# Optimization experiments

Measured on AMD Instinct MI355X. Metric: run time of the kernel, lower is better.

## Reference

```python
import jax, jax.numpy as jnp
import numpy as np

N_SAMPLES = 32768
DAMPING = 0.9998
EPS = 1e-8


def sim(home, tensions, masses, gains, mics, forces, home_modifier):
    # forces, home_modifier: (B, M, D, T); home: (1,1,D,1)
    B, M, D, T = forces.shape
    h = home + home_modifier                          # (B,M,D,T)
    f_t = jnp.moveaxis(forces, -1, 0)                 # (T,B,M,D)
    h_t = jnp.moveaxis(h, -1, 0)                      # (T,B,M,D)

    def step(carry, xs):
        pos, vel = carry
        f, hh = xs
        direction = hh - pos
        acc = f + tensions * direction / masses
        vel = (vel + acc) * DAMPING
        pos = pos + vel
        # mic readout: tanh(vel*gains) dotted with mics over dim
        r = jnp.sum(jnp.tanh(vel * gains) * mics, axis=-1)  # (B,M)
        return (pos, vel), (r, direction)

    init = (jnp.zeros((B, M, D), forces.dtype), jnp.zeros((B, M, D), forces.dtype))
    _, (rec, disp) = jax.lax.scan(step, init, (f_t, h_t))
    recording = jnp.moveaxis(rec, 0, -1)              # (B,M,T)
    displacement = jnp.moveaxis(disp, 0, -1)          # (B,M,D,T)
    return recording, displacement


def interpolate_last_axis(x, size):
    # linear interpolation along last axis (F.interpolate mode='linear', align_corners=False)
    T = x.shape[-1]
    pos = jnp.clip((jnp.arange(size) + 0.5) * (T / size) - 0.5, 0.0, T - 1)
    i0 = jnp.floor(pos).astype(jnp.int32)
    i1 = jnp.minimum(i0 + 1, T - 1)
    w = (pos - i0).astype(x.dtype)
    return x[..., i0] * (1 - w) + x[..., i1] * w


def fft_resample(x, desired):
    # zero-pad spectrum to upsample
    spec = jnp.fft.rfft(x, axis=-1, norm='ortho')
    n_coeffs = desired // 2 + 1
    new = jnp.zeros(x.shape[:-1] + (n_coeffs,), dtype=spec.dtype)
    new = new.at[..., :spec.shape[-1]].set(spec)
    return jnp.fft.irfft(new, n=desired, axis=-1, norm='ortho')


def fft_convolve(a, b):
    # linear convolution via 2N-padded FFT, truncated to N
    n = a.shape[-1]
    pa = jnp.pad(a, [(0, 0)] * (a.ndim - 1) + [(0, n)])
    pb = jnp.pad(b, [(0, 0)] * (b.ndim - 1) + [(0, b.shape[-1])])
    spec = jnp.fft.rfft(pa, axis=-1) * jnp.fft.rfft(pb, axis=-1)
    return jnp.fft.irfft(spec, axis=-1)[..., :n]


def forward(forces, home_modifier, filters, home, masses, tensions, gains, mics, to_filter_mixture):
    recording, displacement = sim(home, tensions, masses, gains, mics, forces, home_modifier)
    mixture = jnp.einsum('bmdt,df->bmft', displacement, to_filter_mixture)
    mixture = interpolate_last_axis(mixture, N_SAMPLES)               # (B,M,F,S)
    upsampled = fft_resample(recording, N_SAMPLES)                    # (B,M,S)
    noise = jax.random.uniform(jax.random.key(1), upsampled.shape,
                               dtype=upsampled.dtype, minval=-1.0, maxval=1.0)
    upsampled = jnp.abs(upsampled) * noise
    f = jnp.pad(filters, ((0, 0), (0, 0), (0, N_SAMPLES - filters.shape[-1])))[:, None, :, :]  # (B,1,F,S)
    f = f / (jnp.linalg.norm(f, axis=-1, keepdims=True) + EPS)
    filtered = fft_convolve(f, upsampled[:, :, None, :])              # (B,M,F,S)
    hf = jnp.einsum('bmfs,bmfs->bms', mixture, filtered) + upsampled  # (B,M,S)
    return recording, displacement, hf


def setup_inputs():
    key = jax.random.key(0)
    ks = jax.random.split(key, 8)
    B, M, D, T, F_, L = 2, 32, 64, 2048, 16, 512
    return {
        'forces': jax.random.normal(ks[0], (B, M, D, T), jnp.float32) * 0.01,
        'home_modifier': jax.random.normal(ks[1], (B, M, D, T), jnp.float32),
        'filters': jax.random.normal(ks[2], (B, F_, L), jnp.float32),
        'home': jnp.zeros((1, 1, D, 1), jnp.float32),
        'masses': jax.random.uniform(ks[3], (1, M, 1), jnp.float32, 1000.0, 10000.0),
        'tensions': jax.random.uniform(ks[4], (1, M, D), jnp.float32, 20.0, 30.0),
        'gains': jax.random.uniform(ks[5], (1, M, 1), jnp.float32, 10.0, 100.0),
        'mics': jax.random.uniform(ks[6], (1, M, D), jnp.float32, -1.0, 1.0),
        'to_filter_mixture': jax.random.uniform(ks[7], (D, F_), jnp.float32, -1.0, 1.0),
    }


def reference(forces, home_modifier, filters, home, masses, tensions, gains, mics, to_filter_mixture):
    return forward(forces, home_modifier, filters, home, masses, tensions, gains, mics, to_filter_mixture)
```

## Files before the change

### kernel.cpp

```cpp
#include <hip/hip_runtime.h>
#include <cstdint>
#include <cstddef>

#define DAMP 0.9998f

typedef __attribute__((ext_vector_type(8))) short bf16x8;
typedef __attribute__((ext_vector_type(4))) float f32x4;

__device__ __forceinline__ unsigned short f2bf(float x) {
    unsigned u = __float_as_uint(x);
    unsigned r = (u + 0x7FFFu + ((u >> 16) & 1u)) >> 16;
    return (unsigned short)r;
}
__device__ __forceinline__ float bf2f(unsigned short v) {
    return __uint_as_float((unsigned)v << 16);
}

__device__ __forceinline__ void threefry_0j(unsigned j, unsigned& o0, unsigned& o1) {
    unsigned x0 = 0u;
    unsigned x1 = j + 1u;
    const unsigned ks2 = 0x1BD11BDBu;
#define TFR(r) { x0 += x1; x1 = (x1 << (r)) | (x1 >> (32 - (r))); x1 ^= x0; }
    TFR(13) TFR(15) TFR(26) TFR(6)
    x0 += 1u;   x1 += ks2 + 1u;
    TFR(17) TFR(29) TFR(16) TFR(24)
    x0 += ks2;  x1 += 0u + 2u;
    TFR(13) TFR(15) TFR(26) TFR(6)
       x1 += 1u + 3u;
    TFR(17) TFR(29) TFR(16) TFR(24)
    x0 += 1u;   x1 += ks2 + 4u;
    TFR(13) TFR(15) TFR(26) TFR(6)
    x0 += ks2;  x1 += 0u + 5u;
#undef TFR
    o0 = x0; o1 = x1;
}

__device__ __forceinline__ float noise_at(unsigned j) {
    unsigned o0, o1;
    threefry_0j(j, o0, o1);
    unsigned bits = o0 ^ o1;
    float u = __uint_as_float((bits >> 9) | 0x3F800000u) - 1.0f;
    return fmaxf(-1.0f, u * 2.0f - 1.0f);
}

__device__ __forceinline__ float dir_val(unsigned u) {
    if (u == 0u) return 2049.f;
    const float PIO = 9.58737992e-05f;
    unsigned y = (2049u * u) & 65535u;
    float sgn = 1.f;
    if (y >= 32768u) { y -= 32768u; sgn = -1.f; }
    unsigned yy = (y > 16384u) ? (32768u - y) : y;
    float sy = sgn * sinf((float)yy * PIO);
    unsigned uu = (u > 16384u) ? (32768u - u) : u;
    float su = sinf((float)uu * PIO);
    return sy / su;
}

__global__ void tables_kernel(const float* __restrict__ filters,
                              unsigned short* __restrict__ dirrev,
                              unsigned short* __restrict__ fnrev) {
    const int tid = threadIdx.x;
    if (blockIdx.x < 128) {
        const unsigned i = blockIdx.x * 256 + tid;
        const unsigned p = i >> 11, k = i & 2047u;
        dirrev[i] = f2bf(dir_val(16u * (2047u - k) + p));
    } else if (tid < 64) {
        const int row = blockIdx.x - 128;
        const float* src = filters + (size_t)row * 512;
        float s = 0.f;
        for (int i = tid; i < 512; i += 64) { const float v = src[i]; s += v * v; }
        #pragma unroll
        for (int off = 32; off; off >>= 1) s += __shfl_xor(s, off);
        const float scale = 1.f / (sqrtf(s) + 1e-8f);
        for (int i = tid; i < 512; i += 64)
            fnrev[(size_t)row * 512 + i] = f2bf(src[511 - i] * scale);
    }
}

__global__ __launch_bounds__(64) void sim_pass1(const float* __restrict__ forces,
                                                const float* __restrict__ hmod,
                                                const float* __restrict__ home,
                                                const float* __restrict__ masses,
                                                const float* __restrict__ tensions,
                                                float* __restrict__ w) {
    const int blk = blockIdx.x;
    const int bm = blk >> 6, c = blk & 63;
    const int m = bm & 31;
    const int d = threadIdx.x;
    const int t0 = c * 32;
    __shared__ float kv[64];
    __shared__ float hv[64];
    __shared__ __align__(16) float gt[64][33];
    kv[d] = tensions[m * 64 + d] / masses[m];
    hv[d] = home[d];
    __syncthreads();
    for (int i = d; i < 512; i += 64) {
        const int dd = i >> 3, q = (i & 7) * 4;
        const size_t off = ((size_t)bm * 64 + dd) * 2048 + t0 + q;
        const float4 fv = *(const float4*)(forces + off);
        const float4 hm = *(const float4*)(hmod + off);
        const float kk = kv[dd], hh = hv[dd];
        float4 g;
        g.x = fmaf(kk, hh + hm.x, fv.x);
        g.y = fmaf(kk, hh + hm.y, fv.y);
        g.z = fmaf(kk, hh + hm.z, fv.z);
        g.w = fmaf(kk, hh + hm.w, fv.w);
        *(float4*)&gt[dd][q] = g;
    }
    __syncthreads();
    const float k = kv[d];
    float pos = 0.f, vel = 0.f;
    #pragma unroll 8
    for (int ts = 0; ts < 32; ++ts) {
        const float acc = fmaf(-k, pos, gt[d][ts]);
        vel = (vel + acc) * DAMP;
        pos = pos + vel;
    }
    float* wrow = w + (size_t)blk * 128;
    wrow[d] = pos; wrow[64 + d] = vel;
}

__global__ __launch_bounds__(64) void sim_scan(const float* __restrict__ masses,
                                               const float* __restrict__ tensions,
                                               float* __restrict__ w) {
    const int bm = blockIdx.x;
    const int m = bm & 31;
    const int d = threadIdx.x;
    const double kd = (double)(tensions[m * 64 + d] / masses[m]);
    const double cd = (double)DAMP;
    double Ma = 1.0 - cd * kd, Mb = cd, Mc = -cd * kd, Md = cd;
    #pragma unroll
    for (int it = 0; it < 5; ++it) {
        const double na = Ma * Ma + Mb * Mc;
        const double nb = Ma * Mb + Mb * Md;
        const double nc = Mc * Ma + Md * Mc;
        const double nd = Mc * Mb + Md * Md;
        Ma = na; Mb = nb; Mc = nc; Md = nd;
    }
    double pos = 0.0, vel = 0.0;
    float* wb = w + (size_t)bm * 64 * 128;
    for (int c = 0; c < 64; ++c) {
        float* row = wb + c * 128;
        const double wp = (double)row[d];
        const double wv = (double)row[64 + d];
        row[d] = (float)pos;
        row[64 + d] = (float)vel;
        const double np = Ma * pos + Mb * vel + wp;
        const double nv = Mc * pos + Md * vel + wv;
        pos = np; vel = nv;
    }
}

__global__ __launch_bounds__(64) void sim_pass2(const float* __restrict__ forces,
                                                const float* __restrict__ hmod,
                                                const float* __restrict__ home,
                                                const float* __restrict__ masses,
                                                const float* __restrict__ tensions,
                                                const float* __restrict__ gains,
                                                const float* __restrict__ mics,
                                                const float* __restrict__ w,
                                                float* __restrict__ disp,
                                                float* __restrict__ rec) {
    const int blk = blockIdx.x;
    const int bm = blk >> 6, c = blk & 63;
    const int m = bm & 31;
    const int d = threadIdx.x;
    const int t0 = c * 32;
    __shared__ __align__(16) float ft[64][17];
    __shared__ __align__(16) float ht[64][17];
    const float k = tensions[m * 64 + d] / masses[m];
    const float gain = gains[m];
    const float mic = mics[m * 64 + d];
    const float hd = home[d];

    float pos = w[(size_t)blk * 128 + d];
    float vel = w[(size_t)blk * 128 + 64 + d];

    #pragma unroll
    for (int phase = 0; phase < 2; ++phase) {
        const int t0p = t0 + phase * 16;
        for (int i = d; i < 256; i += 64) {
            const int dd = i >> 2, q = (i & 3) * 4;
            const size_t off = ((size_t)bm * 64 + dd) * 2048 + t0p + q;
            *(float4*)&ft[dd][q] = *(const float4*)(forces + off);
            *(float4*)&ht[dd][q] = *(const float4*)(hmod + off);
        }
        __syncthreads();
        #pragma unroll
        for (int ts = 0; ts < 16; ++ts) {
            const float f = ft[d][ts];
            const float h = hd + ht[d][ts];
            const float dir = h - pos;
            const float acc = f + k * dir;
            vel = (vel + acc) * DAMP;
            pos = pos + vel;
            ft[d][ts] = dir;
            const float x = vel * gain;
            const float e = __expf(2.f * x);
            ht[d][ts] = (1.f - 2.f / (e + 1.f)) * mic;
        }
        __syncthreads();
        for (int i = d; i < 256; i += 64) {
            const int dd = i >> 2, q = (i & 3) * 4;
            const size_t off = ((size_t)bm * 64 + dd) * 2048 + t0p + q;
            *(float4*)(disp + off) = *(float4*)&ft[dd][q];
        }
        {
            const int ts = d & 15, part = d >> 4;
            float s = 0.f;
            #pragma unroll
            for (int j = 0; j < 16; ++j) s += ht[16 * part + j][ts];
            s += __shfl_xor(s, 16);
            s += __shfl_xor(s, 32);
            if (d < 16) rec[(size_t)bm * 2048 + t0p + d] = s;
        }
        __syncthreads();
    }
}

__global__ __launch_bounds__(256) void mix_kernel(const float* __restrict__ disp,
                                                  const float* __restrict__ tofm,
                                                  unsigned short* __restrict__ mixture) {
    __shared__ __align__(16) float tf[64][16];
    const int tid = threadIdx.x;
    for (int i = tid; i < 1024; i += 256) tf[i >> 4][i & 15] = tofm[i];
    __syncthreads();
    const int bm = blockIdx.y;
    const int t = blockIdx.x * 256 + tid;
    float acc[16];
    #pragma unroll
    for (int f = 0; f < 16; ++f) acc[f] = 0.f;
    for (int d = 0; d < 64; ++d) {
        const float v = disp[((size_t)bm * 64 + d) * 2048 + t];
        const float4* r4 = (const float4*)tf[d];
        const float4 a4 = r4[0], b4 = r4[1], c4 = r4[2], d4 = r4[3];
        acc[0]  += v * a4.x; acc[1]  += v * a4.y; acc[2]  += v * a4.z; acc[3]  += v * a4.w;
        acc[4]  += v * b4.x; acc[5]  += v * b4.y; acc[6]  += v * b4.z; acc[7]  += v * b4.w;
        acc[8]  += v * c4.x; acc[9]  += v * c4.y; acc[10] += v * c4.z; acc[11] += v * c4.w;
        acc[12] += v * d4.x; acc[13] += v * d4.y; acc[14] += v * d4.z; acc[15] += v * d4.w;
    }
    #pragma unroll
    for (int f = 0; f < 16; ++f)
        mixture[((size_t)bm * 16 + f) * 2048 + t] = f2bf(acc[f]);
}

#define DR_STRIDE 4112u
#define W_STRIDE  5136u
#define W_OFF     65792u
#define RS_SMEM   106880u

__global__ __launch_bounds__(256) void resample_kernel(const float* __restrict__ rec,
                                                       const unsigned short* __restrict__ dirrev,
                                                       float* __restrict__ up) {
    const int bm = blockIdx.x;
    const int Q0 = blockIdx.y * 512;
    const int tid = threadIdx.x;
    __shared__ __align__(16) unsigned char smem[RS_SMEM];

    for (int i = tid; i < 4096; i += 256) {
        const int p = i >> 8, c16 = i & 255;
        *(uint4*)(smem + (unsigned)p * DR_STRIDE + 16u * c16) = ((const uint4*)dirrev)[i];
    }
    for (int x = tid; x < 2560; x += 256) {
        const int g = (Q0 + x + 1) & 2047;
        const unsigned short bv = f2bf(rec[(size_t)bm * 2048 + g]);
        #pragma unroll
        for (int sg = 0; sg < 8; ++sg) {
            const int y = x - sg;
            if (y >= 0) *(unsigned short*)(smem + W_OFF + sg * W_STRIDE + 2 * y) = bv;
        }
    }
    __syncthreads();

    const int lane = tid & 63;
    const int wv = tid >> 6;
    const int i15 = lane & 15;
    const int g4 = lane >> 4;

    f32x4 acc[8];
    #pragma unroll
    for (int i = 0; i < 8; ++i) acc[i] = (f32x4){0.f, 0.f, 0.f, 0.f};

    const unsigned abase = (unsigned)i15 * DR_STRIDE + 16u * g4;
    const unsigned bbase = W_OFF + (unsigned)(i15 & 7) * W_STRIDE + 16u * (i15 >> 3) + 16u * g4;

    for (int kkb = 0; kkb < 8; ++kkb) {
        bf16x8 afr[8];
        #pragma unroll
        for (int kj = 0; kj < 8; ++kj)
            afr[kj] = *(const bf16x8*)(smem + abase + 64u * (kkb * 8 + kj));
        #pragma unroll
        for (int qtl = 0; qtl < 8; ++qtl) {
            const int qt = wv * 8 + qtl;
            const unsigned bb = bbase + 32u * qt;
            #pragma unroll
            for (int kj = 0; kj < 8; ++kj) {
                const bf16x8 bfr = *(const bf16x8*)(smem + bb + 64u * (kkb * 8 + kj));
                acc[qtl] = __builtin_amdgcn_mfma_f32_16x16x32_bf16(afr[kj], bfr, acc[qtl], 0, 0, 0);
            }
        }
    }

    #pragma unroll
    for (int qtl = 0; qtl < 8; ++qtl) {
        const int qt = wv * 8 + qtl;
        const int q = Q0 + 16 * qt + i15;
        const int sbase = 16 * q + 4 * g4;
        const unsigned jb = (unsigned)bm * 32768u + (unsigned)sbase;
        float4 o;
        o.x = fabsf(acc[qtl][0] * (1.f / 8192.f)) * noise_at(jb);
        o.y = fabsf(acc[qtl][1] * (1.f / 8192.f)) * noise_at(jb + 1u);
        o.z = fabsf(acc[qtl][2] * (1.f / 8192.f)) * noise_at(jb + 2u);
        o.w = fabsf(acc[qtl][3] * (1.f / 8192.f)) * noise_at(jb + 3u);
        *(float4*)(up + (size_t)bm * 32768 + sbase) = o;
    }
}

#define W_STR2   3088u
#define MX_OFF   24704u
#define HF_SMEM  26880u

__global__ __launch_bounds__(256) void hf_kernel(const float* __restrict__ up,
                                                 const unsigned short* __restrict__ fnrev,
                                                 const unsigned short* __restrict__ mixture,
                                                 float* __restrict__ hf) {
    const int tile = blockIdx.x;
    const int bm = blockIdx.y;
    const int b = bm >> 5;
    const int S0 = tile * 1024;
    const int tbase = tile * 64 - 1;
    const int tid = threadIdx.x;

    __shared__ __align__(16) unsigned char smem[HF_SMEM];
    unsigned short* mixl = (unsigned short*)(smem + MX_OFF);

    for (int x = tid; x < 1536; x += 256) {
        const int gidx = S0 - 511 + x;
        const float u = (gidx >= 0 && gidx < 32768) ? up[(size_t)bm * 32768 + gidx] : 0.f;
        const unsigned short v = f2bf(u);
        #pragma unroll
        for (int sg = 0; sg < 8; ++sg) {
            const int y = x - sg;
            if (y >= 0) *(unsigned short*)(smem + sg * W_STR2 + 2 * y) = v;
        }
    }
    for (int i = tid; i < 16 * 66; i += 256) {
        const int f = i / 66, tt = i - f * 66;
        const int t = tbase + tt;
        mixl[f * 68 + tt] = (t >= 0 && t < 2048)
            ? mixture[((size_t)bm * 16 + f) * 2048 + t] : (unsigned short)0;
    }
    const int lane = tid & 63;
    const int i15 = lane & 15;
    const int g4 = lane >> 4;
    const int wv = tid >> 6;
    bf16x8 afr[16];
    #pragma unroll
    for (int kk = 0; kk < 16; ++kk)
        afr[kk] = *(const bf16x8*)(fnrev + (size_t)(b * 16 + i15) * 512 + 32 * kk + 8 * g4);
    __syncthreads();

    for (int rr = 0; rr < 4; ++rr) {
        const int rho = wv * 4 + rr;
        const int sig = rho & 7;
        const unsigned baseR = (unsigned)sig * W_STR2 + 2u * (rho - sig)
                             + 32u * i15 + 16u * g4;
        #pragma unroll
        for (int g = 0; g < 4; ++g) {
            f32x4 acc = {0.f, 0.f, 0.f, 0.f};
            const unsigned tb = baseR + 512u * g;
            #pragma unroll
            for (int kk = 0; kk < 16; ++kk) {
                const bf16x8 bfr = *(const bf16x8*)(smem + tb + 64u * kk);
                acc = __builtin_amdgcn_mfma_f32_16x16x32_bf16(afr[kk], bfr, acc, 0, 0, 0);
            }
            const int s = S0 + 256 * g + rho + 16 * i15;
            float posf = ((float)s + 0.5f) * 0.0625f - 0.5f;
            posf = fminf(fmaxf(posf, 0.f), 2047.f);
            const int i0 = (int)posf;
            const float wg = posf - (float)i0;
            const int i1 = min(i0 + 1, 2047);
            const int t0 = i0 - tbase, t1 = i1 - tbase;
            float part = 0.f;
            #pragma unroll
            for (int r = 0; r < 4; ++r) {
                const int f = 4 * g4 + r;
                const float mv = bf2f(mixl[f * 68 + t0]) * (1.f - wg)
                               + bf2f(mixl[f * 68 + t1]) * wg;
                part += mv * acc[r];
            }
            part += __shfl_xor(part, 16);
            part += __shfl_xor(part, 32);
            if (g4 == 0) {
                const int e = 511 + 256 * g + rho + 16 * i15;
                const float upv = bf2f(*(const unsigned short*)(smem + 2 * e));
                hf[(size_t)bm * 32768 + s] = part + upv;
            }
        }
    }
}

extern "C" void kernel_launch(void* const* d_in, const int* in_sizes, int n_in,
                              void* d_out, int out_size, void* d_ws, size_t ws_size,
                              hipStream_t stream) {
    const float* forces   = (const float*)d_in[0];
    const float* hmod     = (const float*)d_in[1];
    const float* filters  = (const float*)d_in[2];
    const float* home     = (const float*)d_in[3];
    const float* masses   = (const float*)d_in[4];
    const float* tensions = (const float*)d_in[5];
    const float* gains    = (const float*)d_in[6];
    const float* mics     = (const float*)d_in[7];
    const float* tofm     = (const float*)d_in[8];

    float* out  = (float*)d_out;
    float* rec  = out;
    float* disp = out + 131072;
    float* hf   = out + 8519680;

    float* up               = (float*)d_ws;
    unsigned short* mixture = (unsigned short*)((float*)d_ws + 2097152);
    unsigned short* dirrev  = (unsigned short*)((float*)d_ws + 3145728);
    float* w                = (float*)d_ws + 3162112;
    unsigned short* fnrev   = (unsigned short*)((float*)d_ws + 3686400);

    tables_kernel<<<160, 256, 0, stream>>>(filters, dirrev, fnrev);
    sim_pass1<<<4096, 64, 0, stream>>>(forces, hmod, home, masses, tensions, w);
    sim_scan<<<64, 64, 0, stream>>>(masses, tensions, w);
    sim_pass2<<<4096, 64, 0, stream>>>(forces, hmod, home, masses, tensions, gains, mics, w, disp, rec);
    mix_kernel<<<dim3(8, 64), 256, 0, stream>>>(disp, tofm, mixture);
    resample_kernel<<<dim3(64, 4), 256, 0, stream>>>(rec, dirrev, up);
    hf_kernel<<<dim3(32, 64), 256, 0, stream>>>(up, fnrev, mixture, hf);
}
```

Before: 129.2 us.

## Fold table kernel into sim_pass1, halve resample smem, store upsampled as bf16

The separate tables kernel is removed and its work (the dirrev table and the normalized reversed filters) is done by extra blocks appended to sim_pass1, saving one launch. resample_kernel now stages the dirrev table in two K-halves, which cuts shared memory from about 107KB to 74KB and may allow more blocks per CU. The upsampled intermediate is written as bf16 instead of fp32, halving its write and read traffic, since hf_kernel converted it to bf16 anyway. The cost is an extra barrier per K-chunk in resample.

```diff
diff --git a/kernel.cpp b/kernel.cpp
--- a/kernel.cpp
+++ b/kernel.cpp
@@ -5,6 +5,7 @@
 #define DAMP 0.9998f
 
 typedef __attribute__((ext_vector_type(8))) short bf16x8;
+typedef __attribute__((ext_vector_type(4))) unsigned short u16x4;
 typedef __attribute__((ext_vector_type(4))) float f32x4;
 
 __device__ __forceinline__ unsigned short f2bf(float x) {
@@ -56,37 +57,37 @@
     return sy / su;
 }
 
-__global__ void tables_kernel(const float* __restrict__ filters,
-                              unsigned short* __restrict__ dirrev,
-                              unsigned short* __restrict__ fnrev) {
-    const int tid = threadIdx.x;
-    if (blockIdx.x < 128) {
-        const unsigned i = blockIdx.x * 256 + tid;
-        const unsigned p = i >> 11, k = i & 2047u;
-        dirrev[i] = f2bf(dir_val(16u * (2047u - k) + p));
-    } else if (tid < 64) {
-        const int row = blockIdx.x - 128;
-        const float* src = filters + (size_t)row * 512;
-        float s = 0.f;
-        for (int i = tid; i < 512; i += 64) { const float v = src[i]; s += v * v; }
-        #pragma unroll
-        for (int off = 32; off; off >>= 1) s += __shfl_xor(s, off);
-        const float scale = 1.f / (sqrtf(s) + 1e-8f);
-        for (int i = tid; i < 512; i += 64)
-            fnrev[(size_t)row * 512 + i] = f2bf(src[511 - i] * scale);
-    }
-}
-
 __global__ __launch_bounds__(64) void sim_pass1(const float* __restrict__ forces,
                                                 const float* __restrict__ hmod,
                                                 const float* __restrict__ home,
                                                 const float* __restrict__ masses,
                                                 const float* __restrict__ tensions,
-                                                float* __restrict__ w) {
+                                                float* __restrict__ w,
+                                                const float* __restrict__ filters,
+                                                unsigned short* __restrict__ dirrev,
+                                                unsigned short* __restrict__ fnrev) {
     const int blk = blockIdx.x;
+    const int d = threadIdx.x;
+    if (blk >= 4608) {
+        const int row = blk - 4608;
+        const float* src = filters + (size_t)row * 512;
+        float s = 0.f;
+        for (int i = d; i < 512; i += 64) { const float v = src[i]; s += v * v; }
+        #pragma unroll
+        for (int off = 32; off; off >>= 1) s += __shfl_xor(s, off);
+        const float scale = 1.f / (sqrtf(s) + 1e-8f);
+        for (int i = d; i < 512; i += 64)
+            fnrev[(size_t)row * 512 + i] = f2bf(src[511 - i] * scale);
+        return;
+    }
+    if (blk >= 4096) {
+        const unsigned i = (unsigned)(blk - 4096) * 64u + (unsigned)d;
+        const unsigned p = i >> 11, k = i & 2047u;
+        dirrev[i] = f2bf(dir_val(16u * (2047u - k) + p));
+        return;
+    }
     const int bm = blk >> 6, c = blk & 63;
     const int m = bm & 31;
-    const int d = threadIdx.x;
     const int t0 = c * 32;
     __shared__ float kv[64];
     __shared__ float hv[64];
@@ -244,23 +245,19 @@
         mixture[((size_t)bm * 16 + f) * 2048 + t] = f2bf(acc[f]);
 }
 
-#define DR_STRIDE 4112u
+#define DR_STRIDE 2064u
 #define W_STRIDE  5136u
-#define W_OFF     65792u
-#define RS_SMEM   106880u
+#define W_OFF     33024u
+#define RS_SMEM   74112u
 
 __global__ __launch_bounds__(256) void resample_kernel(const float* __restrict__ rec,
                                                        const unsigned short* __restrict__ dirrev,
-                                                       float* __restrict__ up) {
+                                                       unsigned short* __restrict__ upb) {
     const int bm = blockIdx.x;
     const int Q0 = blockIdx.y * 512;
     const int tid = threadIdx.x;
     __shared__ __align__(16) unsigned char smem[RS_SMEM];
 
-    for (int i = tid; i < 4096; i += 256) {
-        const int p = i >> 8, c16 = i & 255;
-        *(uint4*)(smem + (unsigned)p * DR_STRIDE + 16u * c16) = ((const uint4*)dirrev)[i];
-    }
     for (int x = tid; x < 2560; x += 256) {
         const int g = (Q0 + x + 1) & 2047;
         const unsigned short bv = f2bf(rec[(size_t)bm * 2048 + g]);
@@ -270,7 +267,6 @@
             if (y >= 0) *(unsigned short*)(smem + W_OFF + sg * W_STRIDE + 2 * y) = bv;
         }
     }
-    __syncthreads();
 
     const int lane = tid & 63;
     const int wv = tid >> 6;
@@ -284,19 +280,29 @@
     const unsigned abase = (unsigned)i15 * DR_STRIDE + 16u * g4;
     const unsigned bbase = W_OFF + (unsigned)(i15 & 7) * W_STRIDE + 16u * (i15 >> 3) + 16u * g4;
 
-    for (int kkb = 0; kkb < 8; ++kkb) {
-        bf16x8 afr[8];
-        #pragma unroll
-        for (int kj = 0; kj < 8; ++kj)
-            afr[kj] = *(const bf16x8*)(smem + abase + 64u * (kkb * 8 + kj));
-        #pragma unroll
-        for (int qtl = 0; qtl < 8; ++qtl) {
-            const int qt = wv * 8 + qtl;
-            const unsigned bb = bbase + 32u * qt;
+    for (int kc = 0; kc < 2; ++kc) {
+        if (kc) __syncthreads();
+        for (int i = tid; i < 2048; i += 256) {
+            const int p = i >> 7, c16 = i & 127;
+            *(uint4*)(smem + (unsigned)p * DR_STRIDE + 16u * c16) =
+                *(const uint4*)(dirrev + (size_t)p * 2048 + kc * 1024 + 8 * c16);
+        }
+        __syncthreads();
+
+        for (int kkb = 0; kkb < 4; ++kkb) {
+            bf16x8 afr[8];
             #pragma unroll
-            for (int kj = 0; kj < 8; ++kj) {
-                const bf16x8 bfr = *(const bf16x8*)(smem + bb + 64u * (kkb * 8 + kj));
-                acc[qtl] = __builtin_amdgcn_mfma_f32_16x16x32_bf16(afr[kj], bfr, acc[qtl], 0, 0, 0);
+            for (int kj = 0; kj < 8; ++kj)
+                afr[kj] = *(const bf16x8*)(smem + abase + 64u * (kkb * 8 + kj));
+            #pragma unroll
+            for (int qtl = 0; qtl < 8; ++qtl) {
+                const int qt = wv * 8 + qtl;
+                const unsigned bb = bbase + 32u * qt + 2048u * kc;
+                #pragma unroll
+                for (int kj = 0; kj < 8; ++kj) {
+                    const bf16x8 bfr = *(const bf16x8*)(smem + bb + 64u * (kkb * 8 + kj));
+                    acc[qtl] = __builtin_amdgcn_mfma_f32_16x16x32_bf16(afr[kj], bfr, acc[qtl], 0, 0, 0);
+                }
             }
         }
     }
@@ -307,12 +313,12 @@
         const int q = Q0 + 16 * qt + i15;
         const int sbase = 16 * q + 4 * g4;
         const unsigned jb = (unsigned)bm * 32768u + (unsigned)sbase;
-        float4 o;
-        o.x = fabsf(acc[qtl][0] * (1.f / 8192.f)) * noise_at(jb);
-        o.y = fabsf(acc[qtl][1] * (1.f / 8192.f)) * noise_at(jb + 1u);
-        o.z = fabsf(acc[qtl][2] * (1.f / 8192.f)) * noise_at(jb + 2u);
-        o.w = fabsf(acc[qtl][3] * (1.f / 8192.f)) * noise_at(jb + 3u);
-        *(float4*)(up + (size_t)bm * 32768 + sbase) = o;
+        u16x4 o;
+        o[0] = f2bf(fabsf(acc[qtl][0] * (1.f / 8192.f)) * noise_at(jb));
+        o[1] = f2bf(fabsf(acc[qtl][1] * (1.f / 8192.f)) * noise_at(jb + 1u));
+        o[2] = f2bf(fabsf(acc[qtl][2] * (1.f / 8192.f)) * noise_at(jb + 2u));
+        o[3] = f2bf(fabsf(acc[qtl][3] * (1.f / 8192.f)) * noise_at(jb + 3u));
+        *(u16x4*)(upb + (size_t)bm * 32768 + sbase) = o;
     }
 }
 
@@ -320,7 +326,7 @@
 #define MX_OFF   24704u
 #define HF_SMEM  26880u
 
-__global__ __launch_bounds__(256) void hf_kernel(const float* __restrict__ up,
+__global__ __launch_bounds__(256) void hf_kernel(const unsigned short* __restrict__ upb,
                                                  const unsigned short* __restrict__ fnrev,
                                                  const unsigned short* __restrict__ mixture,
                                                  float* __restrict__ hf) {
@@ -336,8 +342,8 @@
 
     for (int x = tid; x < 1536; x += 256) {
         const int gidx = S0 - 511 + x;
-        const float u = (gidx >= 0 && gidx < 32768) ? up[(size_t)bm * 32768 + gidx] : 0.f;
-        const unsigned short v = f2bf(u);
+        const unsigned short v = (gidx >= 0) ? upb[(size_t)bm * 32768 + gidx]
+                                             : (unsigned short)0;
         #pragma unroll
         for (int sg = 0; sg < 8; ++sg) {
             const int y = x - sg;
@@ -418,17 +424,17 @@
     float* disp = out + 131072;
     float* hf   = out + 8519680;
 
-    float* up               = (float*)d_ws;
-    unsigned short* mixture = (unsigned short*)((float*)d_ws + 2097152);
-    unsigned short* dirrev  = (unsigned short*)((float*)d_ws + 3145728);
-    float* w                = (float*)d_ws + 3162112;
-    unsigned short* fnrev   = (unsigned short*)((float*)d_ws + 3686400);
-
-    tables_kernel<<<160, 256, 0, stream>>>(filters, dirrev, fnrev);
-    sim_pass1<<<4096, 64, 0, stream>>>(forces, hmod, home, masses, tensions, w);
+    unsigned short* upb     = (unsigned short*)d_ws;
+    unsigned short* mixture = (unsigned short*)((float*)d_ws + 1048576);
+    unsigned short* dirrev  = (unsigned short*)((float*)d_ws + 2097152);
+    float* w                = (float*)d_ws + 2113536;
+    unsigned short* fnrev   = (unsigned short*)((float*)d_ws + 2637824);
+
+    sim_pass1<<<4640, 64, 0, stream>>>(forces, hmod, home, masses, tensions, w,
+                                       filters, dirrev, fnrev);
     sim_scan<<<64, 64, 0, stream>>>(masses, tensions, w);
     sim_pass2<<<4096, 64, 0, stream>>>(forces, hmod, home, masses, tensions, gains, mics, w, disp, rec);
     mix_kernel<<<dim3(8, 64), 256, 0, stream>>>(disp, tofm, mixture);
-    resample_kernel<<<dim3(64, 4), 256, 0, stream>>>(rec, dirrev, up);
-    hf_kernel<<<dim3(32, 64), 256, 0, stream>>>(up, fnrev, mixture, hf);
-}
+    resample_kernel<<<dim3(64, 4), 256, 0, stream>>>(rec, dirrev, upb);
+    hf_kernel<<<dim3(32, 64), 256, 0, stream>>>(upb, fnrev, mixture, hf);
+}
```

New measurement: 122.1 us. -5.5%, faster.
